# Kernel optimization log

Measured on AMD Instinct MI355X. Metric: run time of the kernel, lower is better.

## Reference

```python
import jax, jax.numpy as jnp
import numpy as np

MARGIN = 0.25
SCALE = 64.0
OP = 1.0 + MARGIN
ON = -MARGIN
DELTA_P = 1.0 - MARGIN
DELTA_N = MARGIN
NEG_FILL = -1e4  # effectively -inf for these logits (|logit| < ~300)

B, D = 8192, 1024
N_IDS = 512


def setup_inputs() -> dict:
    key = jax.random.key(0)
    k1, k2 = jax.random.split(key)
    inputs = jax.random.normal(k1, (B, D), dtype=jnp.float32)
    targets = jax.random.randint(k2, (B,), 0, N_IDS, dtype=jnp.int64)
    return {"inputs": inputs, "targets": targets}


def reference(inputs, targets):
    # L2-normalize embeddings (torch F.normalize uses eps=1e-12 clamp on norm)
    norm = jnp.maximum(jnp.linalg.norm(inputs, axis=1, keepdims=True), 1e-12)
    x = inputs / norm
    sim = x @ x.T  # [B, B] cosine similarities

    same = targets[:, None] == targets[None, :]
    eye = jnp.eye(targets.shape[0], dtype=bool)
    pos_mask = same & ~eye
    neg_mask = ~same

    sim_sg = jax.lax.stop_gradient(sim)  # .detach() in original
    ap = jnp.maximum(OP - sim_sg, 0.0)
    an = jnp.maximum(sim_sg - ON, 0.0)

    logit_p = -ap * (sim - DELTA_P) * SCALE
    logit_n = an * (sim - DELTA_N) * SCALE

    lse_p = jax.nn.logsumexp(jnp.where(pos_mask, logit_p, NEG_FILL), axis=1)
    lse_n = jax.nn.logsumexp(jnp.where(neg_mask, logit_n, NEG_FILL), axis=1)

    loss_i = jax.nn.softplus(lse_n + lse_p)  # [B]
    valid = pos_mask.any(axis=1) & neg_mask.any(axis=1)

    total = jnp.sum(jnp.where(valid, loss_i, 0.0))
    count = jnp.maximum(jnp.sum(valid), 1)
    return total / count
```

## Files before the change

### kernel.cpp

```cpp
#include <hip/hip_runtime.h>
#include <hip/hip_bf16.h>
#include <math.h>

#define THREADS 256
#define MTHREADS 512
typedef unsigned short ushortT;
typedef __attribute__((ext_vector_type(8))) short bf16x8;
typedef __attribute__((ext_vector_type(4))) float f32x4;

__device__ __forceinline__ void async16(const ushortT* g, ushortT* l) {
  __builtin_amdgcn_global_load_lds(
      (const __attribute__((address_space(1))) unsigned int*)g,
      (__attribute__((address_space(3))) unsigned int*)l, 16, 0, 0);
}

__device__ __forceinline__ ushortT f2bf(float f) {
  __hip_bfloat16 h = __float2bfloat16(f);
  return *reinterpret_cast<ushortT*>(&h);
}

__global__ __launch_bounds__(THREADS) void k_prep(const float* __restrict__ x,
                                                  ushortT* __restrict__ xn, int D) {
  __shared__ float red[4];
  const int row = blockIdx.x;
  const int tid = threadIdx.x;
  const int gid = row * (D / 4) + tid;
  const float4 v = reinterpret_cast<const float4*>(x)[gid];
  float s = v.x * v.x + v.y * v.y + v.z * v.z + v.w * v.w;
  #pragma unroll
  for (int off = 32; off; off >>= 1) s += __shfl_xor(s, off);
  if ((tid & 63) == 0) red[tid >> 6] = s;
  __syncthreads();
  const float tot = red[0] + red[1] + red[2] + red[3];
  const float rn = 1.0f / fmaxf(sqrtf(tot), 1e-12f);
  ushort4 o;
  o.x = f2bf(v.x * rn); o.y = f2bf(v.y * rn);
  o.z = f2bf(v.z * rn); o.w = f2bf(v.w * rn);
  reinterpret_cast<ushort4*>(xn)[gid] = o;
}

__global__ __launch_bounds__(MTHREADS, 2) void k_main_mfma(const ushortT* __restrict__ xn,
                                                           const int* __restrict__ tgt,
                                                           float4* __restrict__ partial,
                                                           int D, int nb) {
  __shared__ ushortT Asm[2][16 * 1024];
  __shared__ ushortT Bsm[2][16 * 1024];

  const int tid = threadIdx.x;
  const int lane = tid & 63;
  const int w = tid >> 6;

  const int b = blockIdx.x;
  int bi = (int)((2.f * nb + 1.f -
                  sqrtf((2.f * nb + 1.f) * (2.f * nb + 1.f) - 8.f * (float)b)) * 0.5f);
  while ((bi + 1) * (2 * nb - bi) / 2 <= b) ++bi;
  while (bi * (2 * nb - bi + 1) / 2 > b) --bi;
  const int bj = bi + (b - bi * (2 * nb - bi + 1) / 2);
  const bool isdiag = (bi == bj);

  const int i0 = bi * 256, j0 = bj * 256;
  const int wr2 = w >> 2;
  const int wc2 = w & 3;
  const int ib = i0 + wr2 * 128;
  const int jb = j0 + wc2 * 64;
  const int nbp = nb * 2;

  const int sr = lane & 15, sc = lane >> 4;
  const ushortT* gA0 = xn + (size_t)(i0 + w * 16 + sr) * D + sc * 8;
  const ushortT* gA1 = gA0 + (size_t)128 * D;
  const ushortT* gB0 = xn + (size_t)(j0 + w * 16 + sr) * D + sc * 8;
  const ushortT* gB1 = gB0 + (size_t)128 * D;

  f32x4 acc[8][4];
  #pragma unroll
  for (int mt = 0; mt < 8; ++mt)
    #pragma unroll
    for (int nt = 0; nt < 4; ++nt)
      acc[mt][nt] = (f32x4){0.f, 0.f, 0.f, 0.f};

  const int kiters = D / 64;
  int cur = 0;

  {
    async16(gA0, &Asm[0][w * 1024]);
    async16(gA0 + 32, &Asm[0][w * 1024 + 512]);
    async16(gA1, &Asm[0][(w + 8) * 1024]);
    async16(gA1 + 32, &Asm[0][(w + 8) * 1024 + 512]);
    async16(gB0, &Bsm[0][w * 1024]);
    async16(gB0 + 32, &Bsm[0][w * 1024 + 512]);
    async16(gB1, &Bsm[0][(w + 8) * 1024]);
    async16(gB1 + 32, &Bsm[0][(w + 8) * 1024 + 512]);
  }
  __syncthreads();

  for (int kk = 0; kk < kiters; ++kk) {
    if (kk + 1 < kiters) {
      const size_t ko = (size_t)(kk + 1) * 64;
      const int nxt = cur ^ 1;
      async16(gA0 + ko, &Asm[nxt][w * 1024]);
      async16(gA0 + ko + 32, &Asm[nxt][w * 1024 + 512]);
      async16(gA1 + ko, &Asm[nxt][(w + 8) * 1024]);
      async16(gA1 + ko + 32, &Asm[nxt][(w + 8) * 1024 + 512]);
      async16(gB0 + ko, &Bsm[nxt][w * 1024]);
      async16(gB0 + ko + 32, &Bsm[nxt][w * 1024 + 512]);
      async16(gB1 + ko, &Bsm[nxt][(w + 8) * 1024]);
      async16(gB1 + ko + 32, &Bsm[nxt][(w + 8) * 1024 + 512]);
    }
    __builtin_amdgcn_sched_barrier(0);
    const ushortT* Ab = Asm[cur];
    const ushortT* Bb = Bsm[cur];
    #pragma unroll 1
    for (int s = 0; s < 2; ++s) {
      bf16x8 bfr[4];
      #pragma unroll
      for (int nt = 0; nt < 4; ++nt)
        bfr[nt] = *reinterpret_cast<const bf16x8*>(&Bb[(wc2 * 4 + nt) * 1024 + s * 512 + lane * 8]);
      #pragma unroll
      for (int mh = 0; mh < 2; ++mh) {
        bf16x8 afr[4];
        #pragma unroll
        for (int t = 0; t < 4; ++t)
          afr[t] = *reinterpret_cast<const bf16x8*>(&Ab[(wr2 * 8 + mh * 4 + t) * 1024 + s * 512 + lane * 8]);
        #pragma unroll
        for (int t = 0; t < 4; ++t)
          #pragma unroll
          for (int nt = 0; nt < 4; ++nt)
            acc[mh * 4 + t][nt] = __builtin_amdgcn_mfma_f32_16x16x32_bf16(afr[t], bfr[nt], acc[mh * 4 + t][nt], 0, 0, 0);
      }
    }
    __syncthreads();
    cur ^= 1;
  }

  const int q = lane >> 4, c = lane & 15;
  int tj[4];
  #pragma unroll
  for (int nt = 0; nt < 4; ++nt) tj[nt] = tgt[jb + nt * 16 + c];

  const int cb1 = bj * 2 + (wc2 >> 1);
  const int half1 = wc2 & 1;
  #pragma unroll
  for (int mt = 0; mt < 8; ++mt) {
    const int4 t4 = *reinterpret_cast<const int4*>(tgt + ib + mt * 16 + q * 4);
    const int tiq[4] = {t4.x, t4.y, t4.z, t4.w};
    #pragma unroll
    for (int reg = 0; reg < 4; ++reg) {
      const int i = ib + mt * 16 + q * 4 + reg;
      const int ti = tiq[reg];
      float m = -1e30f, sn = 0.f;
      #pragma unroll
      for (int nt = 0; nt < 4; ++nt) {
        const float s = acc[mt][nt][reg];
        const int j = jb + nt * 16 + c;
        const bool same = (tj[nt] == ti);
        const bool vpos = same && (j != i);
        const float lp = (fminf(s, 1.25f) - 1.25f) * fmaf(s, 64.f, -48.f);
        m = fmaxf(m, vpos ? lp : -2e30f);
        const float ln = (fmaxf(s, -0.25f) + 0.25f) * fmaf(s, 64.f, -16.f);
        const float en = __expf(ln);
        sn += same ? 0.f : en;
      }
      #pragma unroll
      for (int off = 1; off < 16; off <<= 1) m = fmaxf(m, __shfl_xor(m, off));
      float sp = 0.f;
      #pragma unroll
      for (int nt = 0; nt < 4; ++nt) {
        const float s = acc[mt][nt][reg];
        const int j = jb + nt * 16 + c;
        const bool same = (tj[nt] == ti);
        const bool vpos = same && (j != i);
        const float lp = (fminf(s, 1.25f) - 1.25f) * fmaf(s, 64.f, -48.f);
        sp += __expf((vpos ? lp : -2e30f) - m);
      }
      #pragma unroll
      for (int off = 1; off < 16; off <<= 1) {
        sp += __shfl_xor(sp, off);
        sn += __shfl_xor(sn, off);
      }
      if (c == 0) {
        float4 o; o.x = m; o.y = sp; o.z = 0.f; o.w = sn;
        partial[((size_t)i * nbp + cb1) * 2 + half1] = o;
      }
    }
  }

  if (!isdiag) {
    const int cb2 = bi * 2 + wr2;
    #pragma unroll
    for (int nt = 0; nt < 4; ++nt) {
      const int jt = tj[nt];
      const int jrow = jb + nt * 16 + c;
      float m = -1e30f, sn = 0.f;
      #pragma unroll
      for (int mt = 0; mt < 8; ++mt) {
        const int4 t4 = *reinterpret_cast<const int4*>(tgt + ib + mt * 16 + q * 4);
        const int tiq[4] = {t4.x, t4.y, t4.z, t4.w};
        #pragma unroll
        for (int reg = 0; reg < 4; ++reg) {
          const float s = acc[mt][nt][reg];
          const bool same = (tiq[reg] == jt);
          const float lp = (fminf(s, 1.25f) - 1.25f) * fmaf(s, 64.f, -48.f);
          m = fmaxf(m, same ? lp : -2e30f);
          const float ln = (fmaxf(s, -0.25f) + 0.25f) * fmaf(s, 64.f, -16.f);
          const float en = __expf(ln);
          sn += same ? 0.f : en;
        }
      }
      m = fmaxf(m, __shfl_xor(m, 16));
      m = fmaxf(m, __shfl_xor(m, 32));
      float sp = 0.f;
      #pragma unroll
      for (int mt = 0; mt < 8; ++mt) {
        const int4 t4 = *reinterpret_cast<const int4*>(tgt + ib + mt * 16 + q * 4);
        const int tiq[4] = {t4.x, t4.y, t4.z, t4.w};
        #pragma unroll
        for (int reg = 0; reg < 4; ++reg) {
          const float s = acc[mt][nt][reg];
          const bool same = (tiq[reg] == jt);
          const float lp = (fminf(s, 1.25f) - 1.25f) * fmaf(s, 64.f, -48.f);
          sp += __expf((same ? lp : -2e30f) - m);
        }
      }
      sp += __shfl_xor(sp, 16); sp += __shfl_xor(sp, 32);
      sn += __shfl_xor(sn, 16); sn += __shfl_xor(sn, 32);
      if (lane < 16) {
        float4 o; o.x = m; o.y = sp; o.z = 0.f; o.w = sn;
        partial[((size_t)jrow * nbp + cb2) * 2 + 0] = o;
        float4 z; z.x = -1e30f; z.y = 0.f; z.z = 0.f; z.w = 0.f;
        partial[((size_t)jrow * nbp + cb2) * 2 + 1] = z;
      }
    }
  }
}

__global__ __launch_bounds__(THREADS) void k_reduce(const float4* __restrict__ partial,
                                                    float* __restrict__ row_loss) {
  const int lane = threadIdx.x & 63;
  const int row = blockIdx.x * 4 + (threadIdx.x >> 6);
  const float4 a = partial[(size_t)row * 128 + lane];
  const float4 b = partial[(size_t)row * 128 + 64 + lane];
  float mp = fmaxf(a.x, b.x);
  float sp = a.y * __expf(a.x - mp) + b.y * __expf(b.x - mp);
  float sn = a.w + b.w;
  #pragma unroll
  for (int off = 1; off < 64; off <<= 1) {
    const float m2 = __shfl_xor(mp, off), s2 = __shfl_xor(sp, off);
    const float nm = fmaxf(mp, m2);
    sp = sp * __expf(mp - nm) + s2 * __expf(m2 - nm);
    mp = nm;
    sn += __shfl_xor(sn, off);
  }
  if (lane == 0) {
    float loss = -1.0f;
    if (sp > 0.f && sn > 0.f) {
      const float z = mp + logf(sp) + logf(sn);
      loss = (z > 0.f) ? (z + log1pf(__expf(-z))) : log1pf(__expf(z));
    }
    row_loss[row] = loss;
  }
}

__global__ __launch_bounds__(THREADS) void k_final(const float* __restrict__ row_loss,
                                                   float* __restrict__ out, int B) {
  __shared__ float ssum[4];
  __shared__ float scnt[4];
  const int tid = threadIdx.x;
  float sum = 0.f, cnt = 0.f;
  for (int i = tid; i < B; i += THREADS) {
    const float l = row_loss[i];
    if (l >= 0.f) { sum += l; cnt += 1.f; }
  }
  #pragma unroll
  for (int off = 32; off; off >>= 1) {
    sum += __shfl_xor(sum, off);
    cnt += __shfl_xor(cnt, off);
  }
  if ((tid & 63) == 0) { ssum[tid >> 6] = sum; scnt[tid >> 6] = cnt; }
  __syncthreads();
  if (tid == 0) {
    float ts = 0.f, tc = 0.f;
    #pragma unroll
    for (int w = 0; w < 4; ++w) { ts += ssum[w]; tc += scnt[w]; }
    out[0] = ts / fmaxf(tc, 1.f);
  }
}

extern "C" void kernel_launch(void* const* d_in, const int* in_sizes, int n_in,
                              void* d_out, int out_size, void* d_ws, size_t ws_size,
                              hipStream_t stream) {
  const float* x = (const float*)d_in[0];
  const int* tgt = (const int*)d_in[1];
  float* out = (float*)d_out;
  const int B = in_sizes[1];
  const int D = in_sizes[0] / B;
  const int nb128 = B / 128;
  const int nb256 = B / 256;

  ushortT* xn = (ushortT*)d_ws;
  float4* partial = (float4*)((char*)d_ws + (size_t)B * D * 2);
  float* row_loss = (float*)((char*)d_ws + (size_t)B * D * 2 + (size_t)B * 2 * nb128 * 16);

  k_prep<<<B, THREADS, 0, stream>>>(x, xn, D);
  k_main_mfma<<<nb256 * (nb256 + 1) / 2, MTHREADS, 0, stream>>>(xn, tgt, partial, D, nb256);
  k_reduce<<<B / 4, THREADS, 0, stream>>>(partial, row_loss);
  k_final<<<1, THREADS, 0, stream>>>(row_loss, out, B);
}
```

Before: 301.7 us.

## Use 16 waves per block with 64x64 per-wave tiles in main MFMA kernel

Doubles the main kernel's block to 1024 threads (16 waves) and halves each wave's output tile from 128x64 to 64x64. Each wave now issues two async loads per operand instead of four, and the column-side partial writes fill both halves directly instead of writing a dummy half. The intent is more waves to hide latency, at the cost of a lower MFMA-to-LDS-read ratio per wave and more barrier participants. It also drops the sched_barrier, and the launch bound of 4 blocks of 1024 threads cannot be met given 128 KB of LDS per block.

```diff
diff --git a/kernel.cpp b/kernel.cpp
--- a/kernel.cpp
+++ b/kernel.cpp
@@ -3,7 +3,7 @@
 #include <math.h>
 
 #define THREADS 256
-#define MTHREADS 512
+#define MTHREADS 1024
 typedef unsigned short ushortT;
 typedef __attribute__((ext_vector_type(8))) short bf16x8;
 typedef __attribute__((ext_vector_type(4))) float f32x4;
@@ -39,7 +39,7 @@
   reinterpret_cast<ushort4*>(xn)[gid] = o;
 }
 
-__global__ __launch_bounds__(MTHREADS, 2) void k_main_mfma(const ushortT* __restrict__ xn,
+__global__ __launch_bounds__(MTHREADS, 4) void k_main_mfma(const ushortT* __restrict__ xn,
                                                            const int* __restrict__ tgt,
                                                            float4* __restrict__ partial,
                                                            int D, int nb) {
@@ -59,21 +59,19 @@
   const bool isdiag = (bi == bj);
 
   const int i0 = bi * 256, j0 = bj * 256;
-  const int wr2 = w >> 2;
-  const int wc2 = w & 3;
-  const int ib = i0 + wr2 * 128;
-  const int jb = j0 + wc2 * 64;
+  const int wr3 = w >> 2;
+  const int wc3 = w & 3;
+  const int ib = i0 + wr3 * 64;
+  const int jb = j0 + wc3 * 64;
   const int nbp = nb * 2;
 
   const int sr = lane & 15, sc = lane >> 4;
-  const ushortT* gA0 = xn + (size_t)(i0 + w * 16 + sr) * D + sc * 8;
-  const ushortT* gA1 = gA0 + (size_t)128 * D;
-  const ushortT* gB0 = xn + (size_t)(j0 + w * 16 + sr) * D + sc * 8;
-  const ushortT* gB1 = gB0 + (size_t)128 * D;
-
-  f32x4 acc[8][4];
-  #pragma unroll
-  for (int mt = 0; mt < 8; ++mt)
+  const ushortT* gA = xn + (size_t)(i0 + w * 16 + sr) * D + sc * 8;
+  const ushortT* gB = xn + (size_t)(j0 + w * 16 + sr) * D + sc * 8;
+
+  f32x4 acc[4][4];
+  #pragma unroll
+  for (int mt = 0; mt < 4; ++mt)
     #pragma unroll
     for (int nt = 0; nt < 4; ++nt)
       acc[mt][nt] = (f32x4){0.f, 0.f, 0.f, 0.f};
@@ -81,52 +79,38 @@
   const int kiters = D / 64;
   int cur = 0;
 
-  {
-    async16(gA0, &Asm[0][w * 1024]);
-    async16(gA0 + 32, &Asm[0][w * 1024 + 512]);
-    async16(gA1, &Asm[0][(w + 8) * 1024]);
-    async16(gA1 + 32, &Asm[0][(w + 8) * 1024 + 512]);
-    async16(gB0, &Bsm[0][w * 1024]);
-    async16(gB0 + 32, &Bsm[0][w * 1024 + 512]);
-    async16(gB1, &Bsm[0][(w + 8) * 1024]);
-    async16(gB1 + 32, &Bsm[0][(w + 8) * 1024 + 512]);
-  }
+  async16(gA, &Asm[0][w * 1024]);
+  async16(gA + 32, &Asm[0][w * 1024 + 512]);
+  async16(gB, &Bsm[0][w * 1024]);
+  async16(gB + 32, &Bsm[0][w * 1024 + 512]);
   __syncthreads();
 
   for (int kk = 0; kk < kiters; ++kk) {
     if (kk + 1 < kiters) {
       const size_t ko = (size_t)(kk + 1) * 64;
       const int nxt = cur ^ 1;
-      async16(gA0 + ko, &Asm[nxt][w * 1024]);
-      async16(gA0 + ko + 32, &Asm[nxt][w * 1024 + 512]);
-      async16(gA1 + ko, &Asm[nxt][(w + 8) * 1024]);
-      async16(gA1 + ko + 32, &Asm[nxt][(w + 8) * 1024 + 512]);
-      async16(gB0 + ko, &Bsm[nxt][w * 1024]);
-      async16(gB0 + ko + 32, &Bsm[nxt][w * 1024 + 512]);
-      async16(gB1 + ko, &Bsm[nxt][(w + 8) * 1024]);
-      async16(gB1 + ko + 32, &Bsm[nxt][(w + 8) * 1024 + 512]);
-    }
-    __builtin_amdgcn_sched_barrier(0);
+      async16(gA + ko, &Asm[nxt][w * 1024]);
+      async16(gA + ko + 32, &Asm[nxt][w * 1024 + 512]);
+      async16(gB + ko, &Bsm[nxt][w * 1024]);
+      async16(gB + ko + 32, &Bsm[nxt][w * 1024 + 512]);
+    }
     const ushortT* Ab = Asm[cur];
     const ushortT* Bb = Bsm[cur];
     #pragma unroll 1
     for (int s = 0; s < 2; ++s) {
+      bf16x8 afr[4];
+      #pragma unroll
+      for (int mt = 0; mt < 4; ++mt)
+        afr[mt] = *reinterpret_cast<const bf16x8*>(&Ab[(wr3 * 4 + mt) * 1024 + s * 512 + lane * 8]);
       bf16x8 bfr[4];
       #pragma unroll
       for (int nt = 0; nt < 4; ++nt)
-        bfr[nt] = *reinterpret_cast<const bf16x8*>(&Bb[(wc2 * 4 + nt) * 1024 + s * 512 + lane * 8]);
-      #pragma unroll
-      for (int mh = 0; mh < 2; ++mh) {
-        bf16x8 afr[4];
+        bfr[nt] = *reinterpret_cast<const bf16x8*>(&Bb[(wc3 * 4 + nt) * 1024 + s * 512 + lane * 8]);
+      #pragma unroll
+      for (int mt = 0; mt < 4; ++mt)
         #pragma unroll
-        for (int t = 0; t < 4; ++t)
-          afr[t] = *reinterpret_cast<const bf16x8*>(&Ab[(wr2 * 8 + mh * 4 + t) * 1024 + s * 512 + lane * 8]);
-        #pragma unroll
-        for (int t = 0; t < 4; ++t)
-          #pragma unroll
-          for (int nt = 0; nt < 4; ++nt)
-            acc[mh * 4 + t][nt] = __builtin_amdgcn_mfma_f32_16x16x32_bf16(afr[t], bfr[nt], acc[mh * 4 + t][nt], 0, 0, 0);
-      }
+        for (int nt = 0; nt < 4; ++nt)
+          acc[mt][nt] = __builtin_amdgcn_mfma_f32_16x16x32_bf16(afr[mt], bfr[nt], acc[mt][nt], 0, 0, 0);
     }
     __syncthreads();
     cur ^= 1;
@@ -137,10 +121,10 @@
   #pragma unroll
   for (int nt = 0; nt < 4; ++nt) tj[nt] = tgt[jb + nt * 16 + c];
 
-  const int cb1 = bj * 2 + (wc2 >> 1);
-  const int half1 = wc2 & 1;
-  #pragma unroll
-  for (int mt = 0; mt < 8; ++mt) {
+  const int cb1 = bj * 2 + (wc3 >> 1);
+  const int half1 = wc3 & 1;
+  #pragma unroll
+  for (int mt = 0; mt < 4; ++mt) {
     const int4 t4 = *reinterpret_cast<const int4*>(tgt + ib + mt * 16 + q * 4);
     const int tiq[4] = {t4.x, t4.y, t4.z, t4.w};
     #pragma unroll
@@ -185,14 +169,15 @@
   }
 
   if (!isdiag) {
-    const int cb2 = bi * 2 + wr2;
+    const int cb2 = bi * 2 + (wr3 >> 1);
+    const int half2 = wr3 & 1;
     #pragma unroll
     for (int nt = 0; nt < 4; ++nt) {
       const int jt = tj[nt];
       const int jrow = jb + nt * 16 + c;
       float m = -1e30f, sn = 0.f;
       #pragma unroll
-      for (int mt = 0; mt < 8; ++mt) {
+      for (int mt = 0; mt < 4; ++mt) {
         const int4 t4 = *reinterpret_cast<const int4*>(tgt + ib + mt * 16 + q * 4);
         const int tiq[4] = {t4.x, t4.y, t4.z, t4.w};
         #pragma unroll
@@ -210,7 +195,7 @@
       m = fmaxf(m, __shfl_xor(m, 32));
       float sp = 0.f;
       #pragma unroll
-      for (int mt = 0; mt < 8; ++mt) {
+      for (int mt = 0; mt < 4; ++mt) {
         const int4 t4 = *reinterpret_cast<const int4*>(tgt + ib + mt * 16 + q * 4);
         const int tiq[4] = {t4.x, t4.y, t4.z, t4.w};
         #pragma unroll
@@ -225,9 +210,7 @@
       sn += __shfl_xor(sn, 16); sn += __shfl_xor(sn, 32);
       if (lane < 16) {
         float4 o; o.x = m; o.y = sp; o.z = 0.f; o.w = sn;
-        partial[((size_t)jrow * nbp + cb2) * 2 + 0] = o;
-        float4 z; z.x = -1e30f; z.y = 0.f; z.z = 0.f; z.w = 0.f;
-        partial[((size_t)jrow * nbp + cb2) * 2 + 1] = z;
+        partial[((size_t)jrow * nbp + cb2) * 2 + half2] = o;
       }
     }
   }
```

After: 277.9 us. 7.9% less time.
